# Performance work log

Hardware: AMD Instinct MI355X
Metric: run time of the kernel (lower is better)

Reference implementation:

```python
import jax, jax.numpy as jnp
import numpy as np

N = 4096      # num_nodes
U = 64        # num_units
IN = 2        # input_dim
DIM = U + IN  # 66
H = 4         # attention heads
ALPHA = 0.2   # leaky slope inside attention scores
SLOPE = 0.01  # nn.LeakyReLU() default for subnet activations
NEG_INF = -9e15


def setup_inputs() -> dict:
    key = jax.random.key(0)
    ks = jax.random.split(key, 20)
    def gn(k, shape, fan):
        return jax.random.normal(k, shape, dtype=jnp.float32) / np.float32(np.sqrt(fan))
    adj = jax.random.randint(ks[2], (N, N), 0, 2, dtype=jnp.int32)
    adj = jnp.maximum(adj, jnp.eye(N, dtype=jnp.int32))  # ensure self-loops
    return {
        "inputs": jax.random.normal(ks[0], (1, N * IN), dtype=jnp.float32),
        "hx": jax.random.normal(ks[1], (1, N, U), dtype=jnp.float32),
        "adj": adj,
        "m1_W": gn(ks[3], (H, DIM, DIM), DIM),
        "m1_a1": gn(ks[4], (H, DIM), DIM),
        "m1_a2": gn(ks[5], (H, DIM), DIM),
        "m1_Wout": gn(ks[6], (H * DIM, DIM), H * DIM),
        "m1_ao1": gn(ks[7], (DIM,), DIM),
        "m1_ao2": gn(ks[8], (DIM,), DIM),
        "m2_W": gn(ks[9], (H, DIM, DIM), DIM),
        "m2_a1": gn(ks[10], (H, DIM), DIM),
        "m2_a2": gn(ks[11], (H, DIM), DIM),
        "m2_Wout": gn(ks[12], (H * DIM, DIM), H * DIM),
        "m2_ao1": gn(ks[13], (DIM,), DIM),
        "m2_ao2": gn(ks[14], (DIM,), DIM),
        "g1_W": gn(ks[15], (DIM, 2 * U), DIM),
        "g1_b": jnp.zeros((2 * U,), dtype=jnp.float32),
        "g2_W": gn(ks[16], (DIM, U), DIM),
        "g2_b": jnp.zeros((U,), dtype=jnp.float32),
    }


def gat_layer(x, W, a1, a2, mask):
    # x: [N,Fin], W: [Fin,Fout], a1/a2: [Fout], mask: [N,N] bool
    h = x @ W                                   # [N,Fout]
    f1 = h @ a1                                 # [N] source term
    f2 = h @ a2                                 # [N] target term
    e = jax.nn.leaky_relu(f1[:, None] + f2[None, :], ALPHA)  # [N,N]
    e = jnp.where(mask, e, NEG_INF)
    attn = jax.nn.softmax(e, axis=-1)
    return attn @ h                             # [N,Fout]


def subnet(x, W, a1, a2, Wout, ao1, ao2, mask):
    # multi-head GAT, concat heads, activation, output GAT layer, activation
    heads = jax.vmap(gat_layer, in_axes=(None, 0, 0, 0, None))(x, W, a1, a2, mask)  # [H,N,DIM]
    hcat = jnp.transpose(heads, (1, 0, 2)).reshape(x.shape[0], -1)                   # [N,H*DIM]
    hcat = jax.nn.leaky_relu(hcat, SLOPE)
    out = gat_layer(hcat, Wout, ao1, ao2, mask)                                      # [N,DIM]
    return jax.nn.leaky_relu(out, SLOPE)


def reference(inputs, hx, adj, m1_W, m1_a1, m1_a2, m1_Wout, m1_ao1, m1_ao2,
              m2_W, m2_a1, m2_a2, m2_Wout, m2_ao1, m2_ao2,
              g1_W, g1_b, g2_W, g2_b):
    mask = adj > 0
    xi = inputs.reshape(N, IN)
    xh = hx.reshape(N, U)
    # _GAT1: concat(inputs, hx) -> GATSubNet1 -> linear -> sigmoid -> split r,u
    x1 = jnp.concatenate([xi, xh], axis=-1)                 # [N,DIM]
    g1 = subnet(x1, m1_W, m1_a1, m1_a2, m1_Wout, m1_ao1, m1_ao2, mask)
    value = jax.nn.sigmoid(g1 @ g1_W + g1_b)                # [N,2U]
    r, u = value[:, :U], value[:, U:]
    # _GAT2: concat(inputs, r*hx) -> GATSubNet2 -> linear -> tanh
    x2 = jnp.concatenate([xi, r * xh], axis=-1)             # [N,DIM]
    g2 = subnet(x2, m2_W, m2_a1, m2_a2, m2_Wout, m2_ao1, m2_ao2, mask)
    c = jnp.tanh(g2 @ g2_W + g2_b)                          # [N,U]
    new_state = u * xh + (1.0 - u) * c
    return new_state.reshape(1, N, U)
```

## Files before the change

kernel.cpp:

```cpp
#include <hip/hip_runtime.h>

constexpr int kN = 4096;
constexpr int kDim = 66;
constexpr int kU = 64;
constexpr float kAlpha = 0.2f;
constexpr float kSlope = 0.01f;
constexpr float kLog2e = 1.44269504f;

typedef _Float16 half8 __attribute__((ext_vector_type(8)));
typedef _Float16 half2t __attribute__((ext_vector_type(2)));
typedef float floatx4 __attribute__((ext_vector_type(4)));

__device__ inline unsigned int fkey(float f){
  unsigned int u = __float_as_uint(f);
  return (u & 0x80000000u) ? ~u : (u | 0x80000000u);
}
__device__ inline float funkey(unsigned int k){
  unsigned int u = (k & 0x80000000u) ? (k ^ 0x80000000u) : ~k;
  return __uint_as_float(u);
}

__global__ void setup_k(const int* __restrict__ adj, unsigned long long* __restrict__ packed,
                        const float* __restrict__ in2, const float* __restrict__ hx,
                        _Float16* __restrict__ x1b, _Float16* __restrict__ x2b,
                        const float* __restrict__ m1W, const float* __restrict__ m1a1, const float* __restrict__ m1a2,
                        const float* __restrict__ m1Wo, const float* __restrict__ m1ao1, const float* __restrict__ m1ao2,
                        const float* __restrict__ m2W, const float* __restrict__ m2a1, const float* __restrict__ m2a2,
                        const float* __restrict__ m2Wo, const float* __restrict__ m2ao1, const float* __restrict__ m2ao2,
                        const float* __restrict__ g1W, const float* __restrict__ g1b,
                        const float* __restrict__ g2W, const float* __restrict__ g2b,
                        _Float16* __restrict__ B1t, _Float16* __restrict__ B1t2,
                        _Float16* __restrict__ B2t, _Float16* __restrict__ B2t2,
                        _Float16* __restrict__ Bgt, _Float16* __restrict__ Bft,
                        unsigned int* __restrict__ fmaxbuf){
  int bb = blockIdx.x, t = threadIdx.x;
  if (bb < 16384){
    int gid = bb * 256 + t;
    unsigned long long m = __ballot(adj[gid] != 0);
    if ((t & 63) == 0) packed[gid >> 6] = m;
    return;
  }
  if (bb < 16384 + 1024){
    int i = (bb - 16384) * 4 + (t >> 6);
    int c = t & 63;
    x1b[(size_t)i * 96 + 2 + c] = (_Float16)hx[(size_t)i * kU + c];
    if (c < 2){
      _Float16 xv = (_Float16)in2[i * 2 + c];
      x1b[(size_t)i * 96 + c] = xv;
      x2b[(size_t)i * 96 + c] = xv;
    }
    if (c < 30){
      x1b[(size_t)i * 96 + 66 + c] = (_Float16)0.f;
      x2b[(size_t)i * 96 + 66 + c] = (_Float16)0.f;
    }
    return;
  }
  int b = bb - (16384 + 1024);
  if (b < 8){
    int m = b & 3;
    const float* W  = (b < 4 ? m1W  : m2W)  + (size_t)m * kDim * kDim;
    const float* a1 = (b < 4 ? m1a1 : m2a1) + m * kDim;
    const float* a2 = (b < 4 ? m1a2 : m2a2) + m * kDim;
    _Float16* Bo = (b < 4 ? B1t : B1t2) + (size_t)m * 80 * 96;
    __shared__ float Ws[kDim * kDim];
    __shared__ float wa1s[kDim], wa2s[kDim];
    for (int z = t; z < kDim * kDim; z += 256) Ws[z] = W[z];
    __syncthreads();
    if (t < kDim){
      float s1 = 0.f, s2 = 0.f;
      for (int d = 0; d < kDim; d++){ float wv = Ws[t * kDim + d]; s1 += wv * a1[d]; s2 += wv * a2[d]; }
      wa1s[t] = s1; wa2s[t] = s2;
    }
    __syncthreads();
    for (int z = t; z < 80 * 96; z += 256){
      int nn = z / 96, k = z % 96;
      float val = 0.f;
      if (k < kDim){
        if (nn < kDim) val = Ws[k * kDim + nn];
        else if (nn == 66) val = wa1s[k];
        else if (nn == 67) val = wa2s[k];
      }
      Bo[z] = (_Float16)val;
    }
  } else if (b < 10){
    const float* Wo  = (b == 8 ? m1Wo  : m2Wo);
    const float* ao1 = (b == 8 ? m1ao1 : m2ao1);
    const float* ao2 = (b == 8 ? m1ao2 : m2ao2);
    _Float16* Bo = (b == 8 ? B2t : B2t2);
    __shared__ float wo1s[264], wo2s[264];
    for (int k = t; k < 264; k += 256){
      float s1 = 0.f, s2 = 0.f;
      for (int d = 0; d < kDim; d++){ float wv = Wo[(size_t)k * kDim + d]; s1 += wv * ao1[d]; s2 += wv * ao2[d]; }
      wo1s[k] = s1; wo2s[k] = s2;
    }
    __syncthreads();
    for (int z = t; z < 80 * 288; z += 256){
      int nn = z / 288, k = z % 288;
      float val = 0.f;
      if (k < 264){
        if (nn < kDim) val = Wo[(size_t)k * kDim + nn];
        else if (nn == 66) val = wo1s[k];
        else if (nn == 67) val = wo2s[k];
      }
      Bo[z] = (_Float16)val;
    }
  } else if (b == 10){
    for (int z = t; z < 128 * 96; z += 256){
      int nn = z / 96, k = z % 96;
      float val = 0.f;
      if (k < kDim) val = g1W[k * 128 + nn];
      else if (k == 66) val = g1b[nn];
      Bgt[z] = (_Float16)val;
    }
  } else {
    if (t < 16) fmaxbuf[t] = 0u;
    for (int z = t; z < 64 * 96; z += 256){
      int nn = z / 96, k = z % 96;
      float val = 0.f;
      if (k < kDim) val = g2W[k * 64 + nn];
      else if (k == 66) val = g2b[nn];
      Bft[z] = (_Float16)val;
    }
  }
}

template<int KSTEPS, int NT>
__device__ __forceinline__ void gemmN(const _Float16* __restrict__ Arow,
                                      const _Float16* __restrict__ Bt, floatx4* acc){
  const int lane = threadIdx.x & 63, q = lane >> 4, n = lane & 15;
  #pragma unroll
  for (int v = 0; v < NT; v++) acc[v] = (floatx4){0.f, 0.f, 0.f, 0.f};
  #pragma unroll
  for (int ks = 0; ks < KSTEPS; ks++){
    half8 af = *(const half8*)&Arow[ks * 32 + q * 8];
    #pragma unroll
    for (int nt = 0; nt < NT; nt++){
      half8 bf = *(const half8*)&Bt[(size_t)(nt * 16 + n) * (KSTEPS * 32) + ks * 32 + q * 8];
      acc[nt] = __builtin_amdgcn_mfma_f32_16x16x32_f16(af, bf, acc[nt], 0, 0, 0);
    }
  }
}

__device__ __forceinline__ void epi0(floatx4* acc, int i0, _Float16* __restrict__ Htc,
                                     float* __restrict__ f1c, float* __restrict__ f2c,
                                     unsigned* __restrict__ fmaxslot){
  const int t = threadIdx.x, w = t >> 6, lane = t & 63, q = lane >> 4, n = lane & 15;
  const int ib = i0 + w * 16 + q * 4;
  float lm = -3e38f;
  #pragma unroll
  for (int nt = 0; nt < 5; nt++){
    int c = nt * 16 + n;
    if (c < kDim){
      union { _Float16 h[4]; uint2 v; } pk;
      pk.h[0] = (_Float16)acc[nt][0]; pk.h[1] = (_Float16)acc[nt][1];
      pk.h[2] = (_Float16)acc[nt][2]; pk.h[3] = (_Float16)acc[nt][3];
      *(uint2*)&Htc[(size_t)c * kN + ib] = pk.v;
    } else if (c == 66){
      float4 fv; fv.x = acc[nt][0] * kLog2e; fv.y = acc[nt][1] * kLog2e;
      fv.z = acc[nt][2] * kLog2e; fv.w = acc[nt][3] * kLog2e;
      *(float4*)&f1c[ib] = fv;
      *(uint2*)&Htc[(size_t)66 * kN + ib] = make_uint2(0x3C003C00u, 0x3C003C00u);
    } else if (c == 67){
      float4 fv; fv.x = acc[nt][0] * kLog2e; fv.y = acc[nt][1] * kLog2e;
      fv.z = acc[nt][2] * kLog2e; fv.w = acc[nt][3] * kLog2e;
      *(float4*)&f2c[ib] = fv;
      lm = fmaxf(fmaxf(fv.x, fv.y), fmaxf(fv.z, fv.w));
      *(uint2*)&Htc[(size_t)67 * kN + ib] = make_uint2(0u, 0u);
    }
  }
  lm = fmaxf(lm, __shfl_xor(lm, 16));
  lm = fmaxf(lm, __shfl_xor(lm, 32));
  if (lane == 3) atomicMax(fmaxslot, fkey(lm));
}

__global__ __launch_bounds__(256) void gemm_ht_k(
    const _Float16* __restrict__ A, const _Float16* __restrict__ Bt,
    _Float16* __restrict__ Ht, float* __restrict__ f1, float* __restrict__ f2,
    unsigned int* __restrict__ fmaxp)
{
  const int m = blockIdx.y;
  const int i0 = blockIdx.x * 64;
  const int w = threadIdx.x >> 6, n = threadIdx.x & 15;
  floatx4 acc[5];
  gemmN<3, 5>(A + (size_t)(i0 + w * 16 + n) * 96, Bt + (size_t)m * 80 * 96, acc);
  epi0(acc, i0, Ht + (size_t)m * 68 * kN, f1 + (size_t)m * kN, f2 + (size_t)m * kN, fmaxp + m);
}

template<int JSPLIT>
__global__ __launch_bounds__(256, 4) void attn_mfma_k(
    const _Float16* __restrict__ Ht, const float* __restrict__ f1,
    const float* __restrict__ f2, const unsigned int* __restrict__ fmaxu,
    const unsigned long long* __restrict__ packed,
    _Float16* __restrict__ paccb)
{
  constexpr int JR = kN / JSPLIT;
  constexpr int NCH = JR / 128;
  const int m = blockIdx.y, js = blockIdx.z;
  const int i0 = blockIdx.x * 64;
  const int t = threadIdx.x;
  const int w = t >> 6, lane = t & 63, q = lane >> 4, n = lane & 15;
  const int i = i0 + w * 16 + n;
  const _Float16* Hg = Ht + (size_t)m * 68 * kN;
  const float* f2m = f2 + (size_t)m * kN;
  const float f1v = f1[(size_t)m * kN + i];
  const float fmx = funkey(fmaxu[m]);
  const float t0 = f1v + fmx;
  const float S = fmaxf(t0, kAlpha * t0);
  const float A1f = __builtin_amdgcn_exp2f(t0 - S);
  const float A2f = __builtin_amdgcn_exp2f(kAlpha * t0 - S);
  const half2t a1p = { (_Float16)A1f, (_Float16)A1f };
  const half2t a2p = { (_Float16)A2f, (_Float16)A2f };

  __shared__ __align__(16) _Float16 HtL[80 * 136];
  __shared__ __align__(16) _Float16 B1h[128], B2h[128];

  for (int z = t; z < 12 * 136; z += 256) HtL[68 * 136 + z] = (_Float16)0.f;

  floatx4 acc[5];
  #pragma unroll
  for (int v = 0; v < 5; v++) acc[v] = (floatx4){0.f, 0.f, 0.f, 0.f};

  const int jbase = js * JR;
  const unsigned long long* prow = packed + (size_t)i * 64;
  for (int ch = 0; ch < NCH; ch++){
    const int j0 = jbase + ch * 128;
    __syncthreads();
    for (int z = t; z < 68 * 16; z += 256){
      int row = z >> 4, c16 = z & 15;
      *(uint4*)&HtL[row * 136 + c16 * 8] = *(const uint4*)&Hg[(size_t)row * kN + j0 + c16 * 8];
    }
    if (t < 128){
      float v = f2m[j0 + t] - fmx;
      B1h[t] = (_Float16)__builtin_amdgcn_exp2f(v);
      B2h[t] = (_Float16)__builtin_amdgcn_exp2f(kAlpha * v);
    }
    __syncthreads();
    unsigned long long w0 = prow[(j0 >> 6)];
    unsigned long long w1 = prow[(j0 >> 6) + 1];
    #pragma unroll
    for (int ks = 0; ks < 4; ks++){
      unsigned long long wsel = (ks < 2) ? w0 : w1;
      unsigned int bits = (unsigned int)((wsel >> ((ks & 1) * 32 + q * 8)) & 0xffull);
      union { uint4 v; unsigned int u[4]; } b1v, b2v;
      b1v.v = *(const uint4*)&B1h[ks * 32 + q * 8];
      b2v.v = *(const uint4*)&B2h[ks * 32 + q * 8];
      union { half8 s; unsigned int u[4]; } af;
      #pragma unroll
      for (int e = 0; e < 4; e++){
        half2t x1 = __builtin_bit_cast(half2t, b1v.u[e]);
        half2t x2 = __builtin_bit_cast(half2t, b2v.u[e]);
        half2t m1 = x1 * a1p;
        half2t m2 = x2 * a2p;
        half2t pm = __builtin_elementwise_max(m1, m2);
        unsigned int mm = (((bits >> (2 * e)) & 1u) ? 0x0000FFFFu : 0u)
                        | (((bits >> (2 * e + 1)) & 1u) ? 0xFFFF0000u : 0u);
        af.u[e] = __builtin_bit_cast(unsigned int, pm) & mm;
      }
      #pragma unroll
      for (int nt = 0; nt < 5; nt++){
        const half8 bf = *(const half8*)&HtL[(nt * 16 + n) * 136 + ks * 32 + q * 8];
        acc[nt] = __builtin_amdgcn_mfma_f32_16x16x32_f16(af.s, bf, acc[nt], 0, 0, 0);
      }
    }
  }
  _Float16* pw = paccb + ((size_t)(m * JSPLIT + js) * kN + (i0 + w * 16)) * 72;
  #pragma unroll
  for (int nt = 0; nt < 5; nt++){
    if (nt < 4 || n < 4){
      #pragma unroll
      for (int r = 0; r < 4; r++)
        pw[(q * 4 + r) * 72 + nt * 16 + n] = (_Float16)acc[nt][r];
    }
  }
}

__global__ __launch_bounds__(256) void combineH_gemmO_k(
    const _Float16* __restrict__ pacc, const _Float16* __restrict__ B2tc,
    _Float16* __restrict__ Htoc, float* __restrict__ fo1c, float* __restrict__ fo2c,
    unsigned int* __restrict__ fmaxslot)
{
  __shared__ __align__(16) _Float16 hcatL[64 * 296];
  const int t = threadIdx.x;
  const int i0 = blockIdx.x * 64;
  {
    const int mm = t >> 6, row = t & 63;
    const _Float16* pb = pacc + ((size_t)(mm * 4) * kN + (i0 + row)) * 72;
    constexpr size_t jstep = (size_t)kN * 72;
    float l = 0.f;
    #pragma unroll
    for (int s = 0; s < 4; s++) l += (float)pb[s * jstep + 66];
    float inv = 1.f / l;
    _Float16* hr = hcatL + row * 296 + mm * 66;
    #pragma unroll
    for (int c8 = 0; c8 < 9; c8++){
      float sv[8] = {0.f,0.f,0.f,0.f,0.f,0.f,0.f,0.f};
      #pragma unroll
      for (int s = 0; s < 4; s++){
        half8 hv = *(const half8*)&pb[s * jstep + c8 * 8];
        #pragma unroll
        for (int e = 0; e < 8; e++) sv[e] += (float)hv[e];
      }
      #pragma unroll
      for (int e = 0; e < 8; e++){
        int c = c8 * 8 + e;
        if (c < kDim){
          float vv = sv[e] * inv;
          vv = fmaxf(vv, kSlope * vv);
          hr[c] = (_Float16)vv;
        }
      }
    }
  }
  for (int z = t; z < 64 * 32; z += 256)
    hcatL[(z >> 5) * 296 + 264 + (z & 31)] = (_Float16)0.f;
  __syncthreads();
  const int w = t >> 6, n = t & 15;
  floatx4 acc[5];
  gemmN<9, 5>(hcatL + (w * 16 + n) * 296, B2tc, acc);
  epi0(acc, i0, Htoc, fo1c, fo2c, fmaxslot);
}

template<int EPI>
__global__ __launch_bounds__(256) void combineO_gemm_k(
    const _Float16* __restrict__ pacc, const _Float16* __restrict__ Btc,
    float* __restrict__ uv, const float* __restrict__ hxp,
    _Float16* __restrict__ x2bp, float* __restrict__ outp)
{
  __shared__ __align__(16) _Float16 gbL[64 * 104];
  const int t = threadIdx.x;
  const int i0 = blockIdx.x * 64;
  {
    const int row = t >> 2, cg = t & 3;
    const _Float16* pb = pacc + (size_t)(i0 + row) * 72;
    constexpr size_t jstep = (size_t)kN * 72;
    float l = 0.f;
    #pragma unroll
    for (int s = 0; s < 16; s++) l += (float)pb[s * jstep + 66];
    float inv = 1.f / l;
    _Float16* gr = gbL + row * 104;
    for (int cc = 0; cc < 17; cc++){
      int c = cg * 17 + cc;
      if (c < kDim){
        float vv = 0.f;
        #pragma unroll
        for (int s = 0; s < 16; s++) vv += (float)pb[s * jstep + c];
        vv *= inv; vv = fmaxf(vv, kSlope * vv);
        gr[c] = (_Float16)vv;
      } else if (c == 66) gr[66] = (_Float16)1.f;
      else if (c == 67) gr[67] = (_Float16)0.f;
    }
    #pragma unroll
    for (int e = 0; e < 9; e++) gr[68 + cg * 9 + e] = (_Float16)0.f;
  }
  __syncthreads();
  const int w = t >> 6, lane = t & 63, q = lane >> 4, n = lane & 15;
  const int ib = i0 + w * 16 + q * 4;
  if constexpr (EPI == 1){
    floatx4 acc[8];
    gemmN<3, 8>(gbL + (w * 16 + n) * 104, Btc, acc);
    #pragma unroll
    for (int nt = 0; nt < 8; nt++){
      int c = nt * 16 + n;
      #pragma unroll
      for (int r = 0; r < 4; r++){
        float v = 1.f / (1.f + __expf(-acc[nt][r]));
        if (c < 64) x2bp[(size_t)(ib + r) * 96 + 2 + c] = (_Float16)(v * hxp[(size_t)(ib + r) * kU + c]);
        else        uv[(size_t)(ib + r) * kU + (c - 64)] = v;
      }
    }
  } else {
    floatx4 acc[4];
    gemmN<3, 4>(gbL + (w * 16 + n) * 104, Btc, acc);
    #pragma unroll
    for (int nt = 0; nt < 4; nt++){
      int c = nt * 16 + n;
      #pragma unroll
      for (int r = 0; r < 4; r++){
        float cc2 = tanhf(acc[nt][r]);
        float u2 = uv[(size_t)(ib + r) * kU + c];
        outp[(size_t)(ib + r) * kU + c] = u2 * hxp[(size_t)(ib + r) * kU + c] + (1.f - u2) * cc2;
      }
    }
  }
}

extern "C" void kernel_launch(void* const* d_in, const int* in_sizes, int n_in,
                              void* d_out, int out_size, void* d_ws, size_t ws_size,
                              hipStream_t stream){
  const float* inputs  = (const float*)d_in[0];
  const float* hx      = (const float*)d_in[1];
  const int*   adj     = (const int*)d_in[2];
  const float* m1_W    = (const float*)d_in[3];
  const float* m1_a1   = (const float*)d_in[4];
  const float* m1_a2   = (const float*)d_in[5];
  const float* m1_Wout = (const float*)d_in[6];
  const float* m1_ao1  = (const float*)d_in[7];
  const float* m1_ao2  = (const float*)d_in[8];
  const float* m2_W    = (const float*)d_in[9];
  const float* m2_a1   = (const float*)d_in[10];
  const float* m2_a2   = (const float*)d_in[11];
  const float* m2_Wout = (const float*)d_in[12];
  const float* m2_ao1  = (const float*)d_in[13];
  const float* m2_ao2  = (const float*)d_in[14];
  const float* g1_W    = (const float*)d_in[15];
  const float* g1_b    = (const float*)d_in[16];
  const float* g2_W    = (const float*)d_in[17];
  const float* g2_b    = (const float*)d_in[18];
  float* out = (float*)d_out;

  char* ws = (char*)d_ws;
  size_t off = 0;
  auto alloc = [&](size_t bytes) -> void* {
    void* p = ws + off;
    off = (off + bytes + 255) & ~(size_t)255;
    return p;
  };
  unsigned long long* packed = (unsigned long long*)alloc((size_t)kN * 64 * 8);
  _Float16* x1b  = (_Float16*)alloc((size_t)kN * 96 * 2);
  _Float16* x2b  = (_Float16*)alloc((size_t)kN * 96 * 2);
  _Float16* Ht   = (_Float16*)alloc((size_t)4 * 68 * kN * 2);
  _Float16* Hto  = (_Float16*)alloc((size_t)68 * kN * 2);
  float* f1   = (float*)alloc((size_t)4 * kN * 4);
  float* f2   = (float*)alloc((size_t)4 * kN * 4);
  float* fo1  = (float*)alloc((size_t)kN * 4);
  float* fo2  = (float*)alloc((size_t)kN * 4);
  unsigned int* fmaxbuf = (unsigned int*)alloc(64);
  float* u    = (float*)alloc((size_t)kN * kU * 4);
  _Float16* pacc = (_Float16*)alloc((size_t)16 * kN * 72 * 2);
  _Float16* B1t  = (_Float16*)alloc((size_t)4 * 80 * 96 * 2);
  _Float16* B1t2 = (_Float16*)alloc((size_t)4 * 80 * 96 * 2);
  _Float16* B2t  = (_Float16*)alloc((size_t)80 * 288 * 2);
  _Float16* B2t2 = (_Float16*)alloc((size_t)80 * 288 * 2);
  _Float16* Bgt  = (_Float16*)alloc((size_t)128 * 96 * 2);
  _Float16* Bft  = (_Float16*)alloc((size_t)64 * 96 * 2);
  (void)ws_size; (void)in_sizes; (void)n_in; (void)out_size;

  setup_k<<<16384 + 1024 + 12, 256, 0, stream>>>(adj, packed, inputs, hx, x1b, x2b,
      m1_W, m1_a1, m1_a2, m1_Wout, m1_ao1, m1_ao2,
      m2_W, m2_a1, m2_a2, m2_Wout, m2_ao1, m2_ao2,
      g1_W, g1_b, g2_W, g2_b,
      B1t, B1t2, B2t, B2t2, Bgt, Bft, fmaxbuf);

  gemm_ht_k<<<dim3(64, 4), 256, 0, stream>>>(x1b, B1t, Ht, f1, f2, fmaxbuf + 0);
  attn_mfma_k<4><<<dim3(64, 4, 4), 256, 0, stream>>>(Ht, f1, f2, fmaxbuf + 0, packed, pacc);
  combineH_gemmO_k<<<64, 256, 0, stream>>>(pacc, B2t, Hto, fo1, fo2, fmaxbuf + 4);
  attn_mfma_k<16><<<dim3(64, 1, 16), 256, 0, stream>>>(Hto, fo1, fo2, fmaxbuf + 4, packed, pacc);
  combineO_gemm_k<1><<<64, 256, 0, stream>>>(pacc, Bgt, u, hx, x2b, nullptr);

  gemm_ht_k<<<dim3(64, 4), 256, 0, stream>>>(x2b, B1t2, Ht, f1, f2, fmaxbuf + 5);
  attn_mfma_k<4><<<dim3(64, 4, 4), 256, 0, stream>>>(Ht, f1, f2, fmaxbuf + 5, packed, pacc);
  combineH_gemmO_k<<<64, 256, 0, stream>>>(pacc, B2t2, Hto, fo1, fo2, fmaxbuf + 9);
  attn_mfma_k<16><<<dim3(64, 1, 16), 256, 0, stream>>>(Hto, fo1, fo2, fmaxbuf + 9, packed, pacc);
  combineO_gemm_k<2><<<64, 256, 0, stream>>>(pacc, Bft, u, hx, nullptr, out);
}
```

Baseline: 322.8 us.

## Register-block attention rows per wave, stream H from global, drop LDS staging

The attention kernel is restructured so each wave handles several 16-row tiles (TPW) and reuses each H fragment across all of them in MFMAs. H fragments now load straight from global memory instead of through a shared-memory tile with two barriers per chunk. Each block processes one contiguous j-range, so the split counts and grids change: the head attention splits j into 8 parts and the output attention into 16. The per-head H layout is padded to 80 rows, and the split buffer is enlarged to match. Separately, the combineO reduction now uses vectorized half8 loads per column tile and shares the softmax denominator through LDS. The costs are more registers per thread (launch bounds lowered to 2 blocks), more partial-sum traffic in combineH, and reads of unwritten padding rows that only land in discarded output columns.

Measured after the change: 364.6 us. +13.0%, slower.

```diff
diff --git a/kernel.cpp b/kernel.cpp
--- a/kernel.cpp
+++ b/kernel.cpp
@@ -183,93 +183,103 @@
   const int w = threadIdx.x >> 6, n = threadIdx.x & 15;
   floatx4 acc[5];
   gemmN<3, 5>(A + (size_t)(i0 + w * 16 + n) * 96, Bt + (size_t)m * 80 * 96, acc);
-  epi0(acc, i0, Ht + (size_t)m * 68 * kN, f1 + (size_t)m * kN, f2 + (size_t)m * kN, fmaxp + m);
-}
-
-template<int JSPLIT>
-__global__ __launch_bounds__(256, 4) void attn_mfma_k(
+  epi0(acc, i0, Ht + (size_t)m * 80 * kN, f1 + (size_t)m * kN, f2 + (size_t)m * kN, fmaxp + m);
+}
+
+template<int TPW, int KSR>
+__global__ __launch_bounds__(256, 2) void attn_mfma_k(
     const _Float16* __restrict__ Ht, const float* __restrict__ f1,
     const float* __restrict__ f2, const unsigned int* __restrict__ fmaxu,
     const unsigned long long* __restrict__ packed,
     _Float16* __restrict__ paccb)
 {
-  constexpr int JR = kN / JSPLIT;
-  constexpr int NCH = JR / 128;
-  const int m = blockIdx.y, js = blockIdx.z;
-  const int i0 = blockIdx.x * 64;
+  constexpr int WJ = KSR * 32;
+  const int m = blockIdx.y;
   const int t = threadIdx.x;
   const int w = t >> 6, lane = t & 63, q = lane >> 4, n = lane & 15;
-  const int i = i0 + w * 16 + n;
-  const _Float16* Hg = Ht + (size_t)m * 68 * kN;
+  const int i0b = blockIdx.x * (TPW * 64);
+  const int wrb = i0b + w * (TPW * 16);
+  const int jbase = blockIdx.z * WJ;
+  const _Float16* Hg = Ht + (size_t)m * 80 * kN;
   const float* f2m = f2 + (size_t)m * kN;
-  const float f1v = f1[(size_t)m * kN + i];
+  const float* f1m = f1 + (size_t)m * kN;
   const float fmx = funkey(fmaxu[m]);
-  const float t0 = f1v + fmx;
-  const float S = fmaxf(t0, kAlpha * t0);
-  const float A1f = __builtin_amdgcn_exp2f(t0 - S);
-  const float A2f = __builtin_amdgcn_exp2f(kAlpha * t0 - S);
-  const half2t a1p = { (_Float16)A1f, (_Float16)A1f };
-  const half2t a2p = { (_Float16)A2f, (_Float16)A2f };
-
-  __shared__ __align__(16) _Float16 HtL[80 * 136];
-  __shared__ __align__(16) _Float16 B1h[128], B2h[128];
-
-  for (int z = t; z < 12 * 136; z += 256) HtL[68 * 136 + z] = (_Float16)0.f;
-
-  floatx4 acc[5];
-  #pragma unroll
-  for (int v = 0; v < 5; v++) acc[v] = (floatx4){0.f, 0.f, 0.f, 0.f};
-
-  const int jbase = js * JR;
-  const unsigned long long* prow = packed + (size_t)i * 64;
-  for (int ch = 0; ch < NCH; ch++){
-    const int j0 = jbase + ch * 128;
-    __syncthreads();
-    for (int z = t; z < 68 * 16; z += 256){
-      int row = z >> 4, c16 = z & 15;
-      *(uint4*)&HtL[row * 136 + c16 * 8] = *(const uint4*)&Hg[(size_t)row * kN + j0 + c16 * 8];
-    }
-    if (t < 128){
-      float v = f2m[j0 + t] - fmx;
-      B1h[t] = (_Float16)__builtin_amdgcn_exp2f(v);
-      B2h[t] = (_Float16)__builtin_amdgcn_exp2f(kAlpha * v);
-    }
-    __syncthreads();
-    unsigned long long w0 = prow[(j0 >> 6)];
-    unsigned long long w1 = prow[(j0 >> 6) + 1];
-    #pragma unroll
-    for (int ks = 0; ks < 4; ks++){
-      unsigned long long wsel = (ks < 2) ? w0 : w1;
-      unsigned int bits = (unsigned int)((wsel >> ((ks & 1) * 32 + q * 8)) & 0xffull);
-      union { uint4 v; unsigned int u[4]; } b1v, b2v;
-      b1v.v = *(const uint4*)&B1h[ks * 32 + q * 8];
-      b2v.v = *(const uint4*)&B2h[ks * 32 + q * 8];
-      union { half8 s; unsigned int u[4]; } af;
+
+  __shared__ __align__(16) _Float16 B1h[WJ], B2h[WJ];
+  for (int z = t; z < WJ; z += 256){
+    float v = f2m[jbase + z] - fmx;
+    B1h[z] = (_Float16)__builtin_amdgcn_exp2f(v);
+    B2h[z] = (_Float16)__builtin_amdgcn_exp2f(kAlpha * v);
+  }
+  __syncthreads();
+
+  half2t a1p[TPW], a2p[TPW];
+  const unsigned long long* prow[TPW];
+  #pragma unroll
+  for (int a = 0; a < TPW; a++){
+    int i = wrb + a * 16 + n;
+    float t0 = f1m[i] + fmx;
+    float S = fmaxf(t0, kAlpha * t0);
+    _Float16 A1 = (_Float16)__builtin_amdgcn_exp2f(t0 - S);
+    _Float16 A2 = (_Float16)__builtin_amdgcn_exp2f(kAlpha * t0 - S);
+    a1p[a] = (half2t){A1, A1};
+    a2p[a] = (half2t){A2, A2};
+    prow[a] = packed + (size_t)i * 64;
+  }
+
+  floatx4 acc[TPW][5];
+  #pragma unroll
+  for (int a = 0; a < TPW; a++)
+    #pragma unroll
+    for (int v = 0; v < 5; v++) acc[a][v] = (floatx4){0.f, 0.f, 0.f, 0.f};
+
+  unsigned long long mw[TPW];
+  #pragma unroll
+  for (int ks = 0; ks < KSR; ks++){
+    if ((ks & 1) == 0){
+      int widx = (jbase >> 6) + (ks >> 1);
+      #pragma unroll
+      for (int a = 0; a < TPW; a++) mw[a] = prow[a][widx];
+    }
+    const unsigned shift = (ks & 1) * 32 + q * 8;
+    const int jo = ks * 32 + q * 8;
+    union { uint4 v; unsigned u[4]; } b1v, b2v;
+    b1v.v = *(const uint4*)&B1h[jo];
+    b2v.v = *(const uint4*)&B2h[jo];
+    union { half8 s; unsigned u[4]; } af[TPW];
+    #pragma unroll
+    for (int a = 0; a < TPW; a++){
+      unsigned bits = (unsigned)((mw[a] >> shift) & 0xffull);
       #pragma unroll
       for (int e = 0; e < 4; e++){
         half2t x1 = __builtin_bit_cast(half2t, b1v.u[e]);
         half2t x2 = __builtin_bit_cast(half2t, b2v.u[e]);
-        half2t m1 = x1 * a1p;
-        half2t m2 = x2 * a2p;
-        half2t pm = __builtin_elementwise_max(m1, m2);
-        unsigned int mm = (((bits >> (2 * e)) & 1u) ? 0x0000FFFFu : 0u)
-                        | (((bits >> (2 * e + 1)) & 1u) ? 0xFFFF0000u : 0u);
-        af.u[e] = __builtin_bit_cast(unsigned int, pm) & mm;
-      }
-      #pragma unroll
-      for (int nt = 0; nt < 5; nt++){
-        const half8 bf = *(const half8*)&HtL[(nt * 16 + n) * 136 + ks * 32 + q * 8];
-        acc[nt] = __builtin_amdgcn_mfma_f32_16x16x32_f16(af.s, bf, acc[nt], 0, 0, 0);
-      }
-    }
-  }
-  _Float16* pw = paccb + ((size_t)(m * JSPLIT + js) * kN + (i0 + w * 16)) * 72;
-  #pragma unroll
-  for (int nt = 0; nt < 5; nt++){
-    if (nt < 4 || n < 4){
-      #pragma unroll
-      for (int r = 0; r < 4; r++)
-        pw[(q * 4 + r) * 72 + nt * 16 + n] = (_Float16)acc[nt][r];
+        half2t pm = __builtin_elementwise_max(x1 * a1p[a], x2 * a2p[a]);
+        unsigned mmk = (((bits >> (2 * e)) & 1u) ? 0x0000FFFFu : 0u)
+                     | (((bits >> (2 * e + 1)) & 1u) ? 0xFFFF0000u : 0u);
+        af[a].u[e] = __builtin_bit_cast(unsigned, pm) & mmk;
+      }
+    }
+    const _Float16* hb = Hg + jbase + jo;
+    #pragma unroll
+    for (int nt = 0; nt < 5; nt++){
+      half8 bf = *(const half8*)&hb[(size_t)(nt * 16 + n) * kN];
+      #pragma unroll
+      for (int a = 0; a < TPW; a++)
+        acc[a][nt] = __builtin_amdgcn_mfma_f32_16x16x32_f16(af[a].s, bf, acc[a][nt], 0, 0, 0);
+    }
+  }
+  const int slice = blockIdx.y * gridDim.z + blockIdx.z;
+  _Float16* pw = paccb + ((size_t)slice * kN + wrb) * 72;
+  #pragma unroll
+  for (int a = 0; a < TPW; a++){
+    #pragma unroll
+    for (int nt = 0; nt < 5; nt++){
+      if (nt < 4 || n < 4){
+        #pragma unroll
+        for (int r = 0; r < 4; r++)
+          pw[(a * 16 + q * 4 + r) * 72 + nt * 16 + n] = (_Float16)acc[a][nt][r];
+      }
     }
   }
 }
@@ -284,18 +294,18 @@
   const int i0 = blockIdx.x * 64;
   {
     const int mm = t >> 6, row = t & 63;
-    const _Float16* pb = pacc + ((size_t)(mm * 4) * kN + (i0 + row)) * 72;
+    const _Float16* pb = pacc + ((size_t)(mm * 8) * kN + (i0 + row)) * 72;
     constexpr size_t jstep = (size_t)kN * 72;
     float l = 0.f;
     #pragma unroll
-    for (int s = 0; s < 4; s++) l += (float)pb[s * jstep + 66];
+    for (int s = 0; s < 8; s++) l += (float)pb[s * jstep + 66];
     float inv = 1.f / l;
     _Float16* hr = hcatL + row * 296 + mm * 66;
     #pragma unroll
     for (int c8 = 0; c8 < 9; c8++){
       float sv[8] = {0.f,0.f,0.f,0.f,0.f,0.f,0.f,0.f};
       #pragma unroll
-      for (int s = 0; s < 4; s++){
+      for (int s = 0; s < 8; s++){
         half8 hv = *(const half8*)&pb[s * jstep + c8 * 8];
         #pragma unroll
         for (int e = 0; e < 8; e++) sv[e] += (float)hv[e];
@@ -327,30 +337,46 @@
     _Float16* __restrict__ x2bp, float* __restrict__ outp)
 {
   __shared__ __align__(16) _Float16 gbL[64 * 104];
+  __shared__ float lds_l[64];
   const int t = threadIdx.x;
   const int i0 = blockIdx.x * 64;
   {
-    const int row = t >> 2, cg = t & 3;
+    const int row = t >> 2, part = t & 3;
     const _Float16* pb = pacc + (size_t)(i0 + row) * 72;
     constexpr size_t jstep = (size_t)kN * 72;
-    float l = 0.f;
-    #pragma unroll
-    for (int s = 0; s < 16; s++) l += (float)pb[s * jstep + 66];
-    float inv = 1.f / l;
+    const int nt_tiles = (part == 0) ? 3 : 2;
+    int tiles[3] = { part, part + 4, 8 };
+    float sums[3][8];
+    #pragma unroll
+    for (int ti = 0; ti < 3; ti++)
+      #pragma unroll
+      for (int e = 0; e < 8; e++) sums[ti][e] = 0.f;
+    for (int s = 0; s < 16; s++){
+      for (int ti = 0; ti < nt_tiles; ti++){
+        half8 hv = *(const half8*)&pb[s * jstep + tiles[ti] * 8];
+        #pragma unroll
+        for (int e = 0; e < 8; e++) sums[ti][e] += (float)hv[e];
+      }
+    }
+    if (part == 0) lds_l[row] = sums[2][2];
+    __syncthreads();
+    float inv = 1.f / lds_l[row];
     _Float16* gr = gbL + row * 104;
-    for (int cc = 0; cc < 17; cc++){
-      int c = cg * 17 + cc;
-      if (c < kDim){
-        float vv = 0.f;
-        #pragma unroll
-        for (int s = 0; s < 16; s++) vv += (float)pb[s * jstep + c];
-        vv *= inv; vv = fmaxf(vv, kSlope * vv);
-        gr[c] = (_Float16)vv;
-      } else if (c == 66) gr[66] = (_Float16)1.f;
-      else if (c == 67) gr[67] = (_Float16)0.f;
-    }
-    #pragma unroll
-    for (int e = 0; e < 9; e++) gr[68 + cg * 9 + e] = (_Float16)0.f;
+    for (int ti = 0; ti < nt_tiles; ti++){
+      int T = tiles[ti];
+      #pragma unroll
+      for (int e = 0; e < 8; e++){
+        int c = T * 8 + e;
+        if (c < kDim){
+          float vv = sums[ti][e] * inv;
+          vv = fmaxf(vv, kSlope * vv);
+          gr[c] = (_Float16)vv;
+        } else if (c == 66) gr[66] = (_Float16)1.f;
+        else if (c == 67) gr[67] = (_Float16)0.f;
+      }
+    }
+    #pragma unroll
+    for (int e = 0; e < 9; e++) gr[68 + part * 9 + e] = (_Float16)0.f;
   }
   __syncthreads();
   const int w = t >> 6, lane = t & 63, q = lane >> 4, n = lane & 15;
@@ -418,15 +444,15 @@
   unsigned long long* packed = (unsigned long long*)alloc((size_t)kN * 64 * 8);
   _Float16* x1b  = (_Float16*)alloc((size_t)kN * 96 * 2);
   _Float16* x2b  = (_Float16*)alloc((size_t)kN * 96 * 2);
-  _Float16* Ht   = (_Float16*)alloc((size_t)4 * 68 * kN * 2);
-  _Float16* Hto  = (_Float16*)alloc((size_t)68 * kN * 2);
+  _Float16* Ht   = (_Float16*)alloc((size_t)4 * 80 * kN * 2);
+  _Float16* Hto  = (_Float16*)alloc((size_t)80 * kN * 2);
   float* f1   = (float*)alloc((size_t)4 * kN * 4);
   float* f2   = (float*)alloc((size_t)4 * kN * 4);
   float* fo1  = (float*)alloc((size_t)kN * 4);
   float* fo2  = (float*)alloc((size_t)kN * 4);
   unsigned int* fmaxbuf = (unsigned int*)alloc(64);
   float* u    = (float*)alloc((size_t)kN * kU * 4);
-  _Float16* pacc = (_Float16*)alloc((size_t)16 * kN * 72 * 2);
+  _Float16* pacc = (_Float16*)alloc((size_t)32 * kN * 72 * 2);
   _Float16* B1t  = (_Float16*)alloc((size_t)4 * 80 * 96 * 2);
   _Float16* B1t2 = (_Float16*)alloc((size_t)4 * 80 * 96 * 2);
   _Float16* B2t  = (_Float16*)alloc((size_t)80 * 288 * 2);
@@ -442,14 +468,14 @@
       B1t, B1t2, B2t, B2t2, Bgt, Bft, fmaxbuf);
 
   gemm_ht_k<<<dim3(64, 4), 256, 0, stream>>>(x1b, B1t, Ht, f1, f2, fmaxbuf + 0);
-  attn_mfma_k<4><<<dim3(64, 4, 4), 256, 0, stream>>>(Ht, f1, f2, fmaxbuf + 0, packed, pacc);
+  attn_mfma_k<4, 16><<<dim3(16, 4, 8), 256, 0, stream>>>(Ht, f1, f2, fmaxbuf + 0, packed, pacc);
   combineH_gemmO_k<<<64, 256, 0, stream>>>(pacc, B2t, Hto, fo1, fo2, fmaxbuf + 4);
-  attn_mfma_k<16><<<dim3(64, 1, 16), 256, 0, stream>>>(Hto, fo1, fo2, fmaxbuf + 4, packed, pacc);
+  attn_mfma_k<2, 8><<<dim3(32, 1, 16), 256, 0, stream>>>(Hto, fo1, fo2, fmaxbuf + 4, packed, pacc);
   combineO_gemm_k<1><<<64, 256, 0, stream>>>(pacc, Bgt, u, hx, x2b, nullptr);
 
   gemm_ht_k<<<dim3(64, 4), 256, 0, stream>>>(x2b, B1t2, Ht, f1, f2, fmaxbuf + 5);
-  attn_mfma_k<4><<<dim3(64, 4, 4), 256, 0, stream>>>(Ht, f1, f2, fmaxbuf + 5, packed, pacc);
+  attn_mfma_k<4, 16><<<dim3(16, 4, 8), 256, 0, stream>>>(Ht, f1, f2, fmaxbuf + 5, packed, pacc);
   combineH_gemmO_k<<<64, 256, 0, stream>>>(pacc, B2t2, Hto, fo1, fo2, fmaxbuf + 9);
-  attn_mfma_k<16><<<dim3(64, 1, 16), 256, 0, stream>>>(Hto, fo1, fo2, fmaxbuf + 9, packed, pacc);
+  attn_mfma_k<2, 8><<<dim3(32, 1, 16), 256, 0, stream>>>(Hto, fo1, fo2, fmaxbuf + 9, packed, pacc);
   combineO_gemm_k<2><<<64, 256, 0, stream>>>(pacc, Bft, u, hx, nullptr, out);
 }
```
